# Kernel tuning notes

Hardware: AMD Instinct MI355X
Metric: run time of the kernel (lower is better)

Reference implementation:

```python
import jax, jax.numpy as jnp
from jax import lax
import numpy as np

EPS = 1e-5  # torch BatchNorm2d default eps


def _conv_bn_relu_pool(x, w, b, g, beta):
    # Conv2d(k=3, pad=1) -> BatchNorm2d (training mode: batch stats, biased var)
    # -> ReLU -> MaxPool2d(2). x: (N, Cin, H, W), w: (Cout, Cin, 3, 3)
    y = lax.conv_general_dilated(x, w, window_strides=(1, 1), padding='SAME',
                                 dimension_numbers=('NCHW', 'OIHW', 'NCHW'))
    y = y + b[None, :, None, None]
    m = y.mean(axis=(0, 2, 3), keepdims=True)
    v = y.var(axis=(0, 2, 3), keepdims=True)  # biased, matches torch normalization
    y = (y - m) * lax.rsqrt(v + EPS)
    y = y * g[None, :, None, None] + beta[None, :, None, None]
    y = jax.nn.relu(y)
    return lax.reduce_window(y, -jnp.inf, lax.max, (1, 1, 2, 2), (1, 1, 2, 2), 'VALID')


def setup_inputs() -> dict:
    key = jax.random.key(0)
    ks = jax.random.split(key, 20)
    B, T, C, H, W = 16, 64, 3, 32, 32
    F_in = 64 * (H // 4) * (W // 4)  # 4096 flattened CNN features per frame
    n = lambda i, shape, s=0.05: jax.random.normal(ks[i], shape, jnp.float32) * s
    return {
        'x_1': jax.random.normal(ks[0], (B, T, C, H, W), jnp.float32),
        'x_2': jax.random.normal(ks[1], (B, T, C, H, W), jnp.float32),
        'conv1_w': n(2, (64, 2 * C, 3, 3)), 'conv1_b': n(3, (64,)),
        'bn1_g': 1.0 + n(4, (64,)), 'bn1_b': n(5, (64,)),
        'conv2_w': n(6, (64, 64, 3, 3)), 'conv2_b': n(7, (64,)),
        'bn2_g': 1.0 + n(8, (64,)), 'bn2_b': n(9, (64,)),
        'R_w': n(10, (100, 400)), 'R_b': n(11, (100,)),
        'Q_w': n(12, (100, F_in + 100)), 'Q_b': n(13, (100,)),
        'O_w': n(14, (128, 400)), 'O_b': n(15, (128,)),
        'fc1_w': n(16, (64, 128)), 'fc1_b': n(17, (64,)),
        'fc2_w': n(18, (1, 64)), 'fc2_b': n(19, (1,)),
    }


def reference(x_1, x_2, conv1_w, conv1_b, bn1_g, bn1_b, conv2_w, conv2_b,
              bn2_g, bn2_b, R_w, R_b, Q_w, Q_b, O_w, O_b,
              fc1_w, fc1_b, fc2_w, fc2_b):
    B, T = x_1.shape[0], x_1.shape[1]
    x = jnp.concatenate([x_1, x_2], axis=2)            # (B, T, 2C, H, W)
    xr = x.reshape((B * T,) + x.shape[2:])             # fold time into batch
    y = _conv_bn_relu_pool(xr, conv1_w, conv1_b, bn1_g, bn1_b)
    y = _conv_bn_relu_pool(y, conv2_w, conv2_b, bn2_g, bn2_b)
    feats = y.reshape(B, T, -1)                        # (B, T, 4096)

    A = jnp.array([0.0, 0.25, 0.5, 0.95], jnp.float32)  # leaky-integrator decays
    Q_SIZE = 100

    def step(Ha, in_t):
        # Ha: (B, 4, 100); in_t: (B, F_in)
        Hf = Ha.reshape(B, -1)                          # (B, 400) = H_Size
        Rt = jnp.tanh(Hf @ R_w.T + R_b)                 # (B, 100)
        Qt = jnp.tanh(jnp.concatenate([in_t, Rt], axis=1) @ Q_w.T + Q_b)  # (B,100)
        Ha_new = A[None, :, None] * Ha + (1.0 - A)[None, :, None] * Qt[:, None, :]
        return Ha_new, None

    Ha0 = jnp.zeros((B, len(A), Q_SIZE), jnp.float32)
    Ha_T, _ = lax.scan(step, Ha0, jnp.swapaxes(feats, 0, 1))  # scan over T

    # only the last-timestep RNN output feeds the head (out[:, -1, :])
    out_last = jnp.tanh(Ha_T.reshape(B, -1) @ O_w.T + O_b)    # (B, 128)
    h = jax.nn.relu(out_last @ fc1_w.T + fc1_b)               # (B, 64)
    return jax.nn.sigmoid(h @ fc2_w.T + fc2_b)                # (B, 1)
```

## Files before the change

kernel.cpp:

```cpp
#include <hip/hip_runtime.h>
#include <math.h>


typedef __attribute__((ext_vector_type(8))) short s8v;
typedef __attribute__((ext_vector_type(4))) float f32x4;

__device__ __forceinline__ unsigned short f2bf(float f) {
  union { float f; unsigned u; } x; x.f = f;
  return (unsigned short)((x.u + 0x7FFFu + ((x.u >> 16) & 1u)) >> 16);
}
__device__ __forceinline__ float bf2f(unsigned short u) {
  union { unsigned u; float f; } x; x.u = ((unsigned)u) << 16; return x.f;
}

__global__ __launch_bounds__(256)
void w1_pack(const float* __restrict__ w1, unsigned short* __restrict__ wB1)
{
  int i = blockIdx.x*256 + threadIdx.x;
  if (i < 6144) {
    int kh = i >> 11, rem = i & 2047, co = rem >> 5, k2 = rem & 31;
    unsigned short v = 0;
    if (k2 < 18) {
      int kw = k2 / 6, ci = k2 - 6*kw;
      v = f2bf(w1[co*54 + ci*9 + kh*3 + kw]);
    }
    wB1[i] = v;
  }
}

__global__ __launch_bounds__(256, 4)
void conv1_mfma(const float* __restrict__ x1, const float* __restrict__ x2,
                const unsigned short* __restrict__ wB1,
                float* __restrict__ part,
                unsigned short* __restrict__ pmax1, unsigned short* __restrict__ pmin1)
{
  __shared__ unsigned xin[3688];
  __shared__ float wred[4][4][16][2];
  const int n = blockIdx.x, tid = threadIdx.x;
  const int w = tid >> 6, lane = tid & 63;
  const int q = lane >> 4, r = lane & 15;

  s8v bf[3][4];
  #pragma unroll
  for (int kh = 0; kh < 3; ++kh)
    #pragma unroll
    for (int t = 0; t < 4; ++t)
      bf[kh][t] = *(const s8v*)&wB1[kh*2048 + (((t<<4)+r)<<5) + (q<<3)];

  #pragma unroll
  for (int k = 0; k < 15; ++k) {
    int i = tid + (k<<8);
    if (i < 3688) xin[i] = 0;
  }
  __syncthreads();
  #pragma unroll
  for (int k = 0; k < 12; ++k) {
    int i = tid + (k<<8);
    int cp = i >> 10, p = i & 1023;
    int y = p >> 5, x = p & 31;
    float lo, hi;
    if (cp == 0)      { lo = x1[n*3072 + p];        hi = x1[n*3072 + 1024 + p]; }
    else if (cp == 1) { lo = x1[n*3072 + 2048 + p]; hi = x2[n*3072 + p];        }
    else              { lo = x2[n*3072 + 1024 + p]; hi = x2[n*3072 + 2048 + p]; }
    xin[(y+1)*108 + (x+1)*3 + cp] = (unsigned)f2bf(lo) | ((unsigned)f2bf(hi) << 16);
  }
  __syncthreads();

  float st[4], sq[4];
  #pragma unroll
  for (int t = 0; t < 4; ++t) { st[t] = 0.f; sq[t] = 0.f; }
  float pmx[4][2], pmn[4][2];

  #pragma unroll 1
  for (int xb = 0; xb < 2; ++xb) {
    const int xbase = xb << 4;
    #pragma unroll 2
    for (int j = 0; j < 8; ++j) {
      const int y = (w << 3) + j;
      f32x4 acc[4];
      #pragma unroll
      for (int t = 0; t < 4; ++t) acc[t] = (f32x4){0.f,0.f,0.f,0.f};
      #pragma unroll
      for (int kh = 0; kh < 3; ++kh) {
        int dw = (y + kh)*108 + 3*(xbase + r) + (q << 2);
        union { unsigned u[4]; s8v v; } af;
        af.u[0] = xin[dw];   af.u[1] = xin[dw+1];
        af.u[2] = xin[dw+2]; af.u[3] = xin[dw+3];
        #pragma unroll
        for (int t = 0; t < 4; ++t)
          acc[t] = __builtin_amdgcn_mfma_f32_16x16x32_bf16(af.v, bf[kh][t], acc[t], 0, 0, 0);
      }
      #pragma unroll
      for (int t = 0; t < 4; ++t) {
        st[t] += acc[t][0]+acc[t][1]+acc[t][2]+acc[t][3];
        sq[t] = fmaf(acc[t][0],acc[t][0], fmaf(acc[t][1],acc[t][1],
                fmaf(acc[t][2],acc[t][2], fmaf(acc[t][3],acc[t][3], sq[t]))));
      }
      if ((j & 1) == 0) {
        #pragma unroll
        for (int t = 0; t < 4; ++t) {
          pmx[t][0] = fmaxf(acc[t][0], acc[t][1]); pmx[t][1] = fmaxf(acc[t][2], acc[t][3]);
          pmn[t][0] = fminf(acc[t][0], acc[t][1]); pmn[t][1] = fminf(acc[t][2], acc[t][3]);
        }
      } else {
        const int py = y >> 1;
        #pragma unroll
        for (int t = 0; t < 4; ++t) {
          int co = (t << 4) + r;
          #pragma unroll
          for (int pp = 0; pp < 2; ++pp) {
            float mx = fmaxf(pmx[t][pp], fmaxf(acc[t][2*pp], acc[t][2*pp+1]));
            float mn = fminf(pmn[t][pp], fminf(acc[t][2*pp], acc[t][2*pp+1]));
            int pxp = (xb << 3) + (q << 1) + pp;
            int o = (((n << 8) + (py << 4) + pxp) << 6) + co;
            pmax1[o] = f2bf(mx);
            pmin1[o] = f2bf(mn);
          }
        }
      }
    }
  }

  #pragma unroll
  for (int t = 0; t < 4; ++t) {
    float s = st[t], ss = sq[t];
    s  += __shfl_xor(s, 16);  s  += __shfl_xor(s, 32);
    ss += __shfl_xor(ss, 16); ss += __shfl_xor(ss, 32);
    if (q == 0) { wred[w][t][r][0] = s; wred[w][t][r][1] = ss; }
  }
  __syncthreads();
  if (tid < 64) {
    float s = 0.f, ss = 0.f;
    #pragma unroll
    for (int wv = 0; wv < 4; ++wv) {
      s  += wred[wv][tid >> 4][tid & 15][0];
      ss += wred[wv][tid >> 4][tid & 15][1];
    }
    part[tid*2048 + n*2]     = s;
    part[tid*2048 + n*2 + 1] = ss;
  }
}

__global__ __launch_bounds__(256)
void bn_finalize(const float* __restrict__ part, const float* __restrict__ g,
                 const float* __restrict__ beta, float inv_cnt, float* __restrict__ bn)
{
  __shared__ float red[8];
  const int c = blockIdx.x, tid = threadIdx.x;
  float s = 0.f, ss = 0.f;
  for (int n = tid; n < 1024; n += 256) {
    s  += part[c*2048 + n*2];
    ss += part[c*2048 + n*2 + 1];
  }
  #pragma unroll
  for (int d = 32; d; d >>= 1) { s += __shfl_xor(s, d); ss += __shfl_xor(ss, d); }
  if ((tid & 63) == 0) { red[(tid>>6)*2] = s; red[(tid>>6)*2+1] = ss; }
  __syncthreads();
  if (tid == 0) {
    float S  = red[0]+red[2]+red[4]+red[6];
    float SS = red[1]+red[3]+red[5]+red[7];
    float m  = S * inv_cnt;
    float var = SS * inv_cnt - m*m;
    float sc = g[c] * rsqrtf(var + 1e-5f);
    bn[c]    = sc;
    bn[64+c] = beta[c] - m*sc;
  }
}

__global__ __launch_bounds__(256)
void w2_pack(const float* __restrict__ w2, unsigned short* __restrict__ wB)
{
  int i = blockIdx.x*256 + threadIdx.x;
  if (i < 36864) {
    int khw = i >> 12, rem = i & 4095, co = rem >> 6, ci = rem & 63;
    int chunk = (ci >> 3) ^ (co & 7);
    wB[khw*4096 + co*64 + chunk*8 + (ci & 7)] = f2bf(w2[co*576 + ci*9 + khw]);
  }
}

__global__ __launch_bounds__(256)
void qw_pack(const float* __restrict__ Qw, unsigned short* __restrict__ qB)
{
  int i = blockIdx.x*256 + threadIdx.x;
  if (i < 458752) {
    int j = i >> 12, k = i & 4095;
    qB[i] = (j < 100) ? f2bf(Qw[j*4196 + k]) : (unsigned short)0;
  }
}

__global__ __launch_bounds__(256)
void conv2_mfma(const unsigned short* __restrict__ pmax1,
                const unsigned short* __restrict__ pmin1,
                const float* __restrict__ bn1,
                const unsigned short* __restrict__ wB,
                float* __restrict__ part,
                unsigned short* __restrict__ pmax2, unsigned short* __restrict__ pmin2)
{
  __shared__ unsigned short xin[324*64];
  __shared__ unsigned short wL[9*64*64];
  __shared__ float wred[4][4][16][2];
  __shared__ float bnL[128];
  const int n = blockIdx.x, tid = threadIdx.x;
  const int w = tid >> 6, lane = tid & 63;
  const int q = lane >> 4, col = lane & 15;

  if (tid < 128) bnL[tid] = bn1[tid];
  {
    const s8v* src = (const s8v*)wB;
    s8v* dst = (s8v*)wL;
    #pragma unroll
    for (int i = 0; i < 18; ++i) dst[tid + (i<<8)] = src[tid + (i<<8)];
  }
  __syncthreads();
  {
    #pragma unroll
    for (int k = 0; k < 11; ++k) {
      int i = tid + (k<<8);
      if (i < 324*8) {
        int L = i >> 3, s = i & 7;
        int y = L / 18, x = L - y*18;
        s8v v = (s8v){0,0,0,0,0,0,0,0};
        if (y >= 1 && y <= 16 && x >= 1 && x <= 16) {
          int idx = (((n<<8) + ((y-1)<<4) + (x-1))<<6) + (s<<3);
          s8v mx = *(const s8v*)&pmax1[idx];
          s8v mn = *(const s8v*)&pmin1[idx];
          #pragma unroll
          for (int e = 0; e < 8; ++e) {
            int ci = (s<<3) + e;
            float sc = bnL[ci], sh = bnL[64+ci];
            float vv = bf2f((unsigned short)(sc >= 0.f ? mx[e] : mn[e]));
            v[e] = (short)f2bf(fmaxf(fmaf(vv, sc, sh), 0.f));
          }
        }
        *(s8v*)((char*)xin + L*128 + (((s ^ (L & 7)) << 4))) = v;
      }
    }
  }
  __syncthreads();

  f32x4 acc[4][4];
  #pragma unroll
  for (int mt = 0; mt < 4; ++mt)
    #pragma unroll
    for (int t = 0; t < 4; ++t)
      acc[mt][t] = (f32x4){0.f,0.f,0.f,0.f};

  const int py0 = w << 2;
  #pragma unroll 1
  for (int khw = 0; khw < 9; ++khw) {
    const int kh = khw / 3, kw = khw - 3*kh;
    const char* wslice = (const char*)wL + khw*8192;
    #pragma unroll
    for (int ks = 0; ks < 2; ++ks) {
      const int chunk = (ks << 2) + q;
      s8v bfrag[4];
      #pragma unroll
      for (int t = 0; t < 4; ++t) {
        int co = (t << 4) + col;
        bfrag[t] = *(const s8v*)(wslice + co*128 + (((chunk ^ (co & 7)) << 4)));
      }
      #pragma unroll
      for (int mt = 0; mt < 4; ++mt) {
        int L = (py0 + mt + kh)*18 + (col + kw);
        s8v afrag = *(const s8v*)((const char*)xin + L*128 + (((chunk ^ (L & 7)) << 4)));
        #pragma unroll
        for (int t = 0; t < 4; ++t)
          acc[mt][t] = __builtin_amdgcn_mfma_f32_16x16x32_bf16(afrag, bfrag[t], acc[mt][t], 0, 0, 0);
      }
    }
  }

  #pragma unroll
  for (int t = 0; t < 4; ++t) {
    float s = 0.f, ss = 0.f;
    #pragma unroll
    for (int mt = 0; mt < 4; ++mt)
      #pragma unroll
      for (int r = 0; r < 4; ++r) {
        float v = acc[mt][t][r];
        s += v; ss = fmaf(v, v, ss);
      }
    s  += __shfl_xor(s, 16);  s  += __shfl_xor(s, 32);
    ss += __shfl_xor(ss, 16); ss += __shfl_xor(ss, 32);
    if (q == 0) { wred[w][t][col][0] = s; wred[w][t][col][1] = ss; }
  }
  __syncthreads();
  if (tid < 64) {
    float s = 0.f, ss = 0.f;
    #pragma unroll
    for (int wv = 0; wv < 4; ++wv) {
      s  += wred[wv][tid >> 4][tid & 15][0];
      ss += wred[wv][tid >> 4][tid & 15][1];
    }
    part[tid*2048 + n*2]     = s;
    part[tid*2048 + n*2 + 1] = ss;
  }

  #pragma unroll
  for (int t = 0; t < 4; ++t) {
    int co = (t << 4) + col;
    #pragma unroll
    for (int mp = 0; mp < 2; ++mp) {
      f32x4 a0 = acc[2*mp][t], a1 = acc[2*mp+1][t];
      float mx0 = fmaxf(fmaxf(a0[0], a0[1]), fmaxf(a1[0], a1[1]));
      float mx1 = fmaxf(fmaxf(a0[2], a0[3]), fmaxf(a1[2], a1[3]));
      float mn0 = fminf(fminf(a0[0], a0[1]), fminf(a1[0], a1[1]));
      float mn1 = fminf(fminf(a0[2], a0[3]), fminf(a1[2], a1[3]));
      int pyp = (w << 1) + mp;
      int base = ((n*64 + co) << 6) + (pyp << 3) + (q << 1);
      pmax2[base] = f2bf(mx0); pmax2[base+1] = f2bf(mx1);
      pmin2[base] = f2bf(mn0); pmin2[base+1] = f2bf(mn1);
    }
  }
}

__global__ __launch_bounds__(256)
void preq_mfma(const unsigned short* __restrict__ pmax2,
               const unsigned short* __restrict__ pmin2,
               const float* __restrict__ bn2,
               const unsigned short* __restrict__ qB,
               float* __restrict__ part)
{
  const int mb = blockIdx.x, ks = blockIdx.y, tid = threadIdx.x;
  const int w = tid >> 6, lane = tid & 63;
  const int q = lane >> 4, col = lane & 15;
  const int m = (mb << 6) + (w << 4) + col;
  const int k00 = ks << 8;

  f32x4 acc[7];
  #pragma unroll
  for (int t = 0; t < 7; ++t) acc[t] = (f32x4){0.f,0.f,0.f,0.f};

  #pragma unroll 2
  for (int kk = 0; kk < 8; ++kk) {
    const int k = k00 + (kk << 5) + (q << 3);
    const int c = k >> 6;
    const float sc = bn2[c], sh = bn2[64 + c];
    s8v mx = *(const s8v*)&pmax2[m*4096 + k];
    s8v mn = *(const s8v*)&pmin2[m*4096 + k];
    s8v a;
    #pragma unroll
    for (int e = 0; e < 8; ++e) {
      float vv = bf2f((unsigned short)(sc >= 0.f ? mx[e] : mn[e]));
      a[e] = (short)f2bf(fmaxf(fmaf(vv, sc, sh), 0.f));
    }
    #pragma unroll
    for (int t = 0; t < 7; ++t) {
      s8v b = *(const s8v*)&qB[(((t << 4) + col) << 12) + k];
      acc[t] = __builtin_amdgcn_mfma_f32_16x16x32_bf16(a, b, acc[t], 0, 0, 0);
    }
  }

  float* dst = part + ks*114688 + ((mb << 6) + (w << 4) + (q << 2))*112;
  #pragma unroll
  for (int t = 0; t < 7; ++t)
    #pragma unroll
    for (int r = 0; r < 4; ++r)
      dst[r*112 + (t << 4) + col] = acc[t][r];
}

__global__ __launch_bounds__(256)
void preq_reduce(const float* __restrict__ part, const float* __restrict__ Qb,
                 float* __restrict__ preQ)
{
  int idx = blockIdx.x*256 + threadIdx.x;
  if (idx < 1024*100) {
    int n = idx / 100, j = idx - n*100;
    float s = Qb[j];
    #pragma unroll
    for (int ks = 0; ks < 16; ++ks) s += part[ks*114688 + n*112 + j];
    preQ[idx] = s;
  }
}

__global__ __launch_bounds__(512, 2)
void rnn_head(const float* __restrict__ preQ, const float* __restrict__ Rw,
              const float* __restrict__ Rb, const float* __restrict__ Qw,
              const float* __restrict__ Ow, const float* __restrict__ Ob,
              const float* __restrict__ f1w, const float* __restrict__ f1b,
              const float* __restrict__ f2w, const float* __restrict__ f2b,
              float* __restrict__ out)
{
  __shared__ __align__(16) float ha[400];
  __shared__ float rt[100];
  __shared__ float qt[100];
  __shared__ float pq[6400];
  __shared__ float rb[100];
  __shared__ __align__(16) float ol[128];
  __shared__ float f1[64];
  const int b = blockIdx.x, tid = threadIdx.x;

  for (int i = tid; i < 6400; i += 512) pq[i] = preQ[b*6400 + i];
  if (tid < 100) rb[tid] = Rb[tid];
  if (tid < 400) ha[tid] = 0.f;

  const int o = tid >> 2, q4 = tid & 3;
  float rw[100], qw[25];
  if (tid < 400) {
    const float* rsrc = &Rw[o*400 + q4*100];
    #pragma unroll
    for (int i = 0; i < 25; ++i) {
      float4 v = *(const float4*)&rsrc[i*4];
      rw[i*4] = v.x; rw[i*4+1] = v.y; rw[i*4+2] = v.z; rw[i*4+3] = v.w;
    }
    const float* qsrc = &Qw[o*4196 + 4096 + q4*25];
    #pragma unroll
    for (int i = 0; i < 25; ++i) qw[i] = qsrc[i];
  }
  const int ja = (tid < 400) ? (tid / 100) : 0;
  const int jq = tid - ja*100;
  const float Aa = (ja==0) ? 0.f : (ja==1) ? 0.25f : (ja==2) ? 0.5f : 0.95f;
  const float Ba = 1.f - Aa;
  __syncthreads();

  for (int t = 0; t < 64; ++t) {
    float racc = 0.f;
    if (tid < 400) {
      const float* hp = &ha[q4*100];
      #pragma unroll
      for (int i = 0; i < 25; ++i) {
        float4 h4 = *(const float4*)&hp[i*4];
        racc = fmaf(rw[i*4], h4.x, racc);
        racc = fmaf(rw[i*4+1], h4.y, racc);
        racc = fmaf(rw[i*4+2], h4.z, racc);
        racc = fmaf(rw[i*4+3], h4.w, racc);
      }
      racc += __shfl_xor(racc, 1);
      racc += __shfl_xor(racc, 2);
      if (q4 == 0) rt[o] = tanhf(racc + rb[o]);
    }
    __syncthreads();
    if (tid < 400) {
      float qacc = 0.f;
      const float* rp = &rt[q4*25];
      #pragma unroll
      for (int i = 0; i < 25; ++i) qacc = fmaf(qw[i], rp[i], qacc);
      qacc += __shfl_xor(qacc, 1);
      qacc += __shfl_xor(qacc, 2);
      if (q4 == 0) qt[o] = tanhf(qacc + pq[t*100 + o]);
    }
    __syncthreads();
    if (tid < 400) ha[tid] = fmaf(Aa, ha[tid], Ba*qt[jq]);
    __syncthreads();
  }

  if (tid < 256) {
    const int j2 = tid >> 1, hh = tid & 1;
    const float* osrc = &Ow[j2*400 + hh*200];
    const float* hp = &ha[hh*200];
    float oacc = 0.f;
    #pragma unroll
    for (int i = 0; i < 50; ++i) {
      float4 w4 = *(const float4*)&osrc[i*4];
      float4 h4 = *(const float4*)&hp[i*4];
      oacc = fmaf(w4.x, h4.x, oacc); oacc = fmaf(w4.y, h4.y, oacc);
      oacc = fmaf(w4.z, h4.z, oacc); oacc = fmaf(w4.w, h4.w, oacc);
    }
    oacc += __shfl_xor(oacc, 1);
    if (hh == 0) ol[j2] = tanhf(oacc + Ob[j2]);
  }
  __syncthreads();
  if (tid < 64) {
    float a = 0.f;
    #pragma unroll
    for (int i = 0; i < 32; ++i) {
      float4 w4 = *(const float4*)&f1w[tid*128 + i*4];
      float4 o4 = *(const float4*)&ol[i*4];
      a = fmaf(w4.x, o4.x, a); a = fmaf(w4.y, o4.y, a);
      a = fmaf(w4.z, o4.z, a); a = fmaf(w4.w, o4.w, a);
    }
    f1[tid] = fmaxf(a + f1b[tid], 0.f);
  }
  __syncthreads();
  if (tid == 0) {
    float a = 0.f;
    for (int i = 0; i < 64; ++i) a = fmaf(f2w[i], f1[i], a);
    out[b] = 1.f / (1.f + expf(-(a + f2b[0])));
  }
}

extern "C" void kernel_launch(void* const* d_in, const int* in_sizes, int n_in,
                              void* d_out, int out_size, void* d_ws, size_t ws_size,
                              hipStream_t stream) {
  (void)in_sizes; (void)n_in; (void)out_size; (void)ws_size;
  const float* x1   = (const float*)d_in[0];
  const float* x2   = (const float*)d_in[1];
  const float* c1w  = (const float*)d_in[2];
  const float* bn1g = (const float*)d_in[4];
  const float* bn1b = (const float*)d_in[5];
  const float* c2w  = (const float*)d_in[6];
  const float* bn2g = (const float*)d_in[8];
  const float* bn2b = (const float*)d_in[9];
  const float* Rw   = (const float*)d_in[10];
  const float* Rb   = (const float*)d_in[11];
  const float* Qw   = (const float*)d_in[12];
  const float* Qb   = (const float*)d_in[13];
  const float* Ow   = (const float*)d_in[14];
  const float* Ob   = (const float*)d_in[15];
  const float* f1w  = (const float*)d_in[16];
  const float* f1b  = (const float*)d_in[17];
  const float* f2w  = (const float*)d_in[18];
  const float* f2b  = (const float*)d_in[19];
  float* outp = (float*)d_out;

  char* wsb = (char*)d_ws;
  unsigned short* pmax1 = (unsigned short*)wsb;
  unsigned short* pmin1 = (unsigned short*)(wsb + 33554432);
  unsigned short* pmax2 = (unsigned short*)(wsb + 67108864);
  unsigned short* pmin2 = (unsigned short*)(wsb + 75497472);
  float* part1  = (float*)(wsb + 83886080);
  float* part2  = part1 + 131072;
  float* bn1    = part2 + 131072;
  float* bn2    = bn1 + 128;
  float* preQ   = bn2 + 128;
  unsigned short* wB1 = (unsigned short*)(preQ + 102400);
  unsigned short* wB2 = wB1 + 6144;
  unsigned short* qB  = wB2 + 36864;
  float* pqpart = (float*)(qB + 458752);

  w1_pack<<<24, 256, 0, stream>>>(c1w, wB1);
  w2_pack<<<144, 256, 0, stream>>>(c2w, wB2);
  qw_pack<<<1792, 256, 0, stream>>>(Qw, qB);
  conv1_mfma<<<1024, 256, 0, stream>>>(x1, x2, wB1, part1, pmax1, pmin1);
  bn_finalize<<<64, 256, 0, stream>>>(part1, bn1g, bn1b, 1.f/1048576.f, bn1);
  conv2_mfma<<<1024, 256, 0, stream>>>(pmax1, pmin1, bn1, wB2, part2, pmax2, pmin2);
  bn_finalize<<<64, 256, 0, stream>>>(part2, bn2g, bn2b, 1.f/262144.f, bn2);
  preq_mfma<<<dim3(16,16), 256, 0, stream>>>(pmax2, pmin2, bn2, qB, pqpart);
  preq_reduce<<<400, 256, 0, stream>>>(pqpart, Qb, preQ);
  rnn_head<<<16, 512, 0, stream>>>(preQ, Rw, Rb, Qw, Ow, Ob, f1w, f1b, f2w, f2b, outp);
}
```

Before: 203.9 us.

## Batch RNN recurrence into single block using bf16 MFMA for R and Q matmuls

Replaces the 16-block per-sequence scalar RNN kernel with one 512-thread block that processes all 16 sequences together. The recurrent R and Q-hidden matmuls now run as 16x16x32 bf16 MFMAs, with packed weights held in registers and the hidden state mirrored as bf16 in LDS. A fast exp/rcp tanh replaces tanhf, and preQ is written time-major so each step's loads are contiguous. The intent is to shorten the 64-step serial latency chain. The cost is bf16 rounding of the recurrent state and weights, an extra packing kernel, and a head that now runs on a single CU.

```diff
diff --git a/kernel.cpp b/kernel.cpp
--- a/kernel.cpp
+++ b/kernel.cpp
@@ -11,6 +11,10 @@
 }
 __device__ __forceinline__ float bf2f(unsigned short u) {
   union { unsigned u; float f; } x; x.u = ((unsigned)u) << 16; return x.f;
+}
+__device__ __forceinline__ float ftanh(float x) {
+  float e = __expf(2.f * x);
+  return 1.f - 2.f * __builtin_amdgcn_rcpf(e + 1.f);
 }
 
 __global__ __launch_bounds__(256)
@@ -189,6 +193,21 @@
 }
 
 __global__ __launch_bounds__(256)
+void rq_pack(const float* __restrict__ Rw, const float* __restrict__ Qw,
+             unsigned short* __restrict__ rB, unsigned short* __restrict__ qrB)
+{
+  int i = blockIdx.x*256 + threadIdx.x;
+  if (i < 46592) {
+    int o = i / 416, k = i - o*416;
+    rB[i] = (o < 100 && k < 400) ? f2bf(Rw[o*400 + k]) : (unsigned short)0;
+  } else if (i < 60928) {
+    int j = i - 46592;
+    int o = j >> 7, kr = j & 127;
+    qrB[j] = (o < 100 && kr < 100) ? f2bf(Qw[o*4196 + 4096 + kr]) : (unsigned short)0;
+  }
+}
+
+__global__ __launch_bounds__(256)
 void conv2_mfma(const unsigned short* __restrict__ pmax1,
                 const unsigned short* __restrict__ pmin1,
                 const float* __restrict__ bn1,
@@ -361,7 +380,7 @@
 
 __global__ __launch_bounds__(256)
 void preq_reduce(const float* __restrict__ part, const float* __restrict__ Qb,
-                 float* __restrict__ preQ)
+                 float* __restrict__ preQ2)
 {
   int idx = blockIdx.x*256 + threadIdx.x;
   if (idx < 1024*100) {
@@ -369,113 +388,151 @@
     float s = Qb[j];
     #pragma unroll
     for (int ks = 0; ks < 16; ++ks) s += part[ks*114688 + n*112 + j];
-    preQ[idx] = s;
-  }
-}
-
-__global__ __launch_bounds__(512, 2)
-void rnn_head(const float* __restrict__ preQ, const float* __restrict__ Rw,
-              const float* __restrict__ Rb, const float* __restrict__ Qw,
-              const float* __restrict__ Ow, const float* __restrict__ Ob,
-              const float* __restrict__ f1w, const float* __restrict__ f1b,
-              const float* __restrict__ f2w, const float* __restrict__ f2b,
-              float* __restrict__ out)
-{
-  __shared__ __align__(16) float ha[400];
-  __shared__ float rt[100];
-  __shared__ float qt[100];
-  __shared__ float pq[6400];
-  __shared__ float rb[100];
-  __shared__ __align__(16) float ol[128];
-  __shared__ float f1[64];
-  const int b = blockIdx.x, tid = threadIdx.x;
-
-  for (int i = tid; i < 6400; i += 512) pq[i] = preQ[b*6400 + i];
-  if (tid < 100) rb[tid] = Rb[tid];
-  if (tid < 400) ha[tid] = 0.f;
-
-  const int o = tid >> 2, q4 = tid & 3;
-  float rw[100], qw[25];
-  if (tid < 400) {
-    const float* rsrc = &Rw[o*400 + q4*100];
-    #pragma unroll
-    for (int i = 0; i < 25; ++i) {
-      float4 v = *(const float4*)&rsrc[i*4];
-      rw[i*4] = v.x; rw[i*4+1] = v.y; rw[i*4+2] = v.z; rw[i*4+3] = v.w;
-    }
-    const float* qsrc = &Qw[o*4196 + 4096 + q4*25];
-    #pragma unroll
-    for (int i = 0; i < 25; ++i) qw[i] = qsrc[i];
-  }
-  const int ja = (tid < 400) ? (tid / 100) : 0;
-  const int jq = tid - ja*100;
-  const float Aa = (ja==0) ? 0.f : (ja==1) ? 0.25f : (ja==2) ? 0.5f : 0.95f;
-  const float Ba = 1.f - Aa;
+    int b = n >> 6, t = n & 63;
+    preQ2[((t << 4) + b)*100 + j] = s;
+  }
+}
+
+__global__ __launch_bounds__(512)
+void rnn_fused(const float* __restrict__ preQ2,
+               const unsigned short* __restrict__ rB,
+               const unsigned short* __restrict__ qrB,
+               const float* __restrict__ Rb,
+               const float* __restrict__ Ow, const float* __restrict__ Ob,
+               const float* __restrict__ f1w, const float* __restrict__ f1b,
+               const float* __restrict__ f2w, const float* __restrict__ f2b,
+               float* __restrict__ out)
+{
+  __shared__ __align__(16) float ha[6400];
+  __shared__ __align__(16) unsigned short haB[16*424];
+  __shared__ __align__(16) unsigned short rtB[16*136];
+  __shared__ float qtL[16*112];
+  __shared__ __align__(16) float olL[16*128];
+  __shared__ __align__(16) float f1L[16*64];
+  const int tid = threadIdx.x;
+  const int w = tid >> 6, lane = tid & 63;
+  const int q = lane >> 4, col = lane & 15;
+  const int o16 = (w << 4) + col;
+
+  s8v rw[13], qw[4];
+  float rbv = 0.f;
+  if (w < 7) {
+    #pragma unroll
+    for (int kk = 0; kk < 13; ++kk)
+      rw[kk] = *(const s8v*)&rB[o16*416 + (kk << 5) + (q << 3)];
+    #pragma unroll
+    for (int kk = 0; kk < 4; ++kk)
+      qw[kk] = *(const s8v*)&qrB[o16*128 + (kk << 5) + (q << 3)];
+    rbv = (o16 < 100) ? Rb[o16] : 0.f;
+  }
+
+  for (int i = tid; i < 6400; i += 512) ha[i] = 0.f;
+  for (int i = tid; i < 16*424; i += 512) haB[i] = 0;
+  for (int i = tid; i < 16*136; i += 512) rtB[i] = 0;
+
+  float A_[13], B_[13];
+  int qo_[13], hb_[13];
+  #pragma unroll
+  for (int j = 0; j < 13; ++j) {
+    int idx = tid + (j << 9);
+    if (idx >= 6400) idx = 6399;
+    int bb = idx / 400; int rem = idx - bb*400;
+    int a = rem / 100;
+    float Aa = (a == 0) ? 0.f : (a == 1) ? 0.25f : (a == 2) ? 0.5f : 0.95f;
+    A_[j] = Aa; B_[j] = 1.f - Aa;
+    qo_[j] = bb*112 + (rem - a*100);
+    hb_[j] = bb*424 + rem;
+  }
   __syncthreads();
 
   for (int t = 0; t < 64; ++t) {
-    float racc = 0.f;
-    if (tid < 400) {
-      const float* hp = &ha[q4*100];
-      #pragma unroll
-      for (int i = 0; i < 25; ++i) {
-        float4 h4 = *(const float4*)&hp[i*4];
-        racc = fmaf(rw[i*4], h4.x, racc);
-        racc = fmaf(rw[i*4+1], h4.y, racc);
-        racc = fmaf(rw[i*4+2], h4.z, racc);
-        racc = fmaf(rw[i*4+3], h4.w, racc);
-      }
-      racc += __shfl_xor(racc, 1);
-      racc += __shfl_xor(racc, 2);
-      if (q4 == 0) rt[o] = tanhf(racc + rb[o]);
+    float pqv[4];
+    if (w < 7) {
+      #pragma unroll
+      for (int r = 0; r < 4; ++r)
+        pqv[r] = (o16 < 100) ? preQ2[((t << 4) + (q << 2) + r)*100 + o16] : 0.f;
+    }
+    if (w < 7) {
+      f32x4 r0 = (f32x4){0.f,0.f,0.f,0.f}, r1 = (f32x4){0.f,0.f,0.f,0.f};
+      #pragma unroll
+      for (int kk = 0; kk < 13; kk += 2) {
+        s8v af = *(const s8v*)&haB[col*424 + (kk << 5) + (q << 3)];
+        r0 = __builtin_amdgcn_mfma_f32_16x16x32_bf16(af, rw[kk], r0, 0, 0, 0);
+        if (kk + 1 < 13) {
+          s8v af2 = *(const s8v*)&haB[col*424 + ((kk+1) << 5) + (q << 3)];
+          r1 = __builtin_amdgcn_mfma_f32_16x16x32_bf16(af2, rw[kk+1], r1, 0, 0, 0);
+        }
+      }
+      #pragma unroll
+      for (int r = 0; r < 4; ++r)
+        rtB[((q << 2) + r)*136 + o16] = f2bf(ftanh(r0[r] + r1[r] + rbv));
     }
     __syncthreads();
-    if (tid < 400) {
-      float qacc = 0.f;
-      const float* rp = &rt[q4*25];
-      #pragma unroll
-      for (int i = 0; i < 25; ++i) qacc = fmaf(qw[i], rp[i], qacc);
-      qacc += __shfl_xor(qacc, 1);
-      qacc += __shfl_xor(qacc, 2);
-      if (q4 == 0) qt[o] = tanhf(qacc + pq[t*100 + o]);
+    if (w < 7) {
+      f32x4 qacc = (f32x4){0.f,0.f,0.f,0.f};
+      #pragma unroll
+      for (int kk = 0; kk < 4; ++kk) {
+        s8v af = *(const s8v*)&rtB[col*136 + (kk << 5) + (q << 3)];
+        qacc = __builtin_amdgcn_mfma_f32_16x16x32_bf16(af, qw[kk], qacc, 0, 0, 0);
+      }
+      #pragma unroll
+      for (int r = 0; r < 4; ++r)
+        qtL[((q << 2) + r)*112 + o16] = ftanh(qacc[r] + pqv[r]);
     }
     __syncthreads();
-    if (tid < 400) ha[tid] = fmaf(Aa, ha[tid], Ba*qt[jq]);
+    #pragma unroll
+    for (int j = 0; j < 13; ++j) {
+      if (j < 12 || tid < 256) {
+        int idx = tid + (j << 9);
+        float hv = fmaf(A_[j], ha[idx], B_[j]*qtL[qo_[j]]);
+        ha[idx] = hv;
+        haB[hb_[j]] = f2bf(hv);
+      }
+    }
     __syncthreads();
   }
 
-  if (tid < 256) {
-    const int j2 = tid >> 1, hh = tid & 1;
-    const float* osrc = &Ow[j2*400 + hh*200];
-    const float* hp = &ha[hh*200];
-    float oacc = 0.f;
-    #pragma unroll
-    for (int i = 0; i < 50; ++i) {
-      float4 w4 = *(const float4*)&osrc[i*4];
-      float4 h4 = *(const float4*)&hp[i*4];
-      oacc = fmaf(w4.x, h4.x, oacc); oacc = fmaf(w4.y, h4.y, oacc);
-      oacc = fmaf(w4.z, h4.z, oacc); oacc = fmaf(w4.w, h4.w, oacc);
-    }
-    oacc += __shfl_xor(oacc, 1);
-    if (hh == 0) ol[j2] = tanhf(oacc + Ob[j2]);
-  }
-  __syncthreads();
-  if (tid < 64) {
-    float a = 0.f;
-    #pragma unroll
-    for (int i = 0; i < 32; ++i) {
-      float4 w4 = *(const float4*)&f1w[tid*128 + i*4];
-      float4 o4 = *(const float4*)&ol[i*4];
-      a = fmaf(w4.x, o4.x, a); a = fmaf(w4.y, o4.y, a);
-      a = fmaf(w4.z, o4.z, a); a = fmaf(w4.w, o4.w, a);
-    }
-    f1[tid] = fmaxf(a + f1b[tid], 0.f);
-  }
-  __syncthreads();
-  if (tid == 0) {
-    float a = 0.f;
-    for (int i = 0; i < 64; ++i) a = fmaf(f2w[i], f1[i], a);
-    out[b] = 1.f / (1.f + expf(-(a + f2b[0])));
+  {
+    const int b = tid >> 5, jb = tid & 31;
+    const float* hp = &ha[b*400];
+    #pragma unroll 1
+    for (int jj = 0; jj < 4; ++jj) {
+      int j = jb + (jj << 5);
+      const float* wp = &Ow[j*400];
+      float a2 = Ob[j];
+      #pragma unroll 4
+      for (int k = 0; k < 400; k += 4) {
+        float4 h4 = *(const float4*)&hp[k];
+        float4 w4 = *(const float4*)&wp[k];
+        a2 = fmaf(h4.x, w4.x, fmaf(h4.y, w4.y, fmaf(h4.z, w4.z, fmaf(h4.w, w4.w, a2))));
+      }
+      olL[b*128 + j] = ftanh(a2);
+    }
+  }
+  __syncthreads();
+  {
+    const int b = tid >> 5, jb = tid & 31;
+    const float* op = &olL[b*128];
+    #pragma unroll 1
+    for (int jj = 0; jj < 2; ++jj) {
+      int j = jb + (jj << 5);
+      const float* wp = &f1w[j*128];
+      float a2 = f1b[j];
+      #pragma unroll 4
+      for (int k = 0; k < 128; k += 4) {
+        float4 o4 = *(const float4*)&op[k];
+        float4 w4 = *(const float4*)&wp[k];
+        a2 = fmaf(o4.x, w4.x, fmaf(o4.y, w4.y, fmaf(o4.z, w4.z, fmaf(o4.w, w4.w, a2))));
+      }
+      f1L[b*64 + j] = fmaxf(a2, 0.f);
+    }
+  }
+  __syncthreads();
+  if (tid < 16) {
+    float a2 = f2b[0];
+    #pragma unroll 8
+    for (int k = 0; k < 64; ++k) a2 = fmaf(f2w[k], f1L[tid*64 + k], a2);
+    out[tid] = __builtin_amdgcn_rcpf(1.f + __expf(-a2));
   }
 }
 
@@ -512,20 +569,23 @@
   float* part2  = part1 + 131072;
   float* bn1    = part2 + 131072;
   float* bn2    = bn1 + 128;
-  float* preQ   = bn2 + 128;
-  unsigned short* wB1 = (unsigned short*)(preQ + 102400);
+  float* preQ2  = bn2 + 128;
+  unsigned short* wB1 = (unsigned short*)(preQ2 + 102400);
   unsigned short* wB2 = wB1 + 6144;
   unsigned short* qB  = wB2 + 36864;
-  float* pqpart = (float*)(qB + 458752);
+  unsigned short* rB  = qB + 458752;
+  unsigned short* qrB = rB + 46592;
+  float* pqpart = (float*)(qrB + 14336);
 
   w1_pack<<<24, 256, 0, stream>>>(c1w, wB1);
   w2_pack<<<144, 256, 0, stream>>>(c2w, wB2);
   qw_pack<<<1792, 256, 0, stream>>>(Qw, qB);
+  rq_pack<<<238, 256, 0, stream>>>(Rw, Qw, rB, qrB);
   conv1_mfma<<<1024, 256, 0, stream>>>(x1, x2, wB1, part1, pmax1, pmin1);
   bn_finalize<<<64, 256, 0, stream>>>(part1, bn1g, bn1b, 1.f/1048576.f, bn1);
   conv2_mfma<<<1024, 256, 0, stream>>>(pmax1, pmin1, bn1, wB2, part2, pmax2, pmin2);
   bn_finalize<<<64, 256, 0, stream>>>(part2, bn2g, bn2b, 1.f/262144.f, bn2);
   preq_mfma<<<dim3(16,16), 256, 0, stream>>>(pmax2, pmin2, bn2, qB, pqpart);
-  preq_reduce<<<400, 256, 0, stream>>>(pqpart, Qb, preQ);
-  rnn_head<<<16, 512, 0, stream>>>(preQ, Rw, Rb, Qw, Ow, Ob, f1w, f1b, f2w, f2b, outp);
-}
+  preq_reduce<<<400, 256, 0, stream>>>(pqpart, Qb, preQ2);
+  rnn_fused<<<1, 512, 0, stream>>>(preQ2, rB, qrB, Rb, Ow, Ob, f1w, f1b, f2w, f2b, outp);
+}
```

New measurement: 270.4 us. 1.33x slower.
